# Kernel optimization log

Measured on AMD Instinct MI355X. Metric: run time of the kernel, lower is better.

## Reference

```python
import jax, jax.numpy as jnp
import numpy as np

B, N, F, H, OUT = 64, 512, 128, 256, 6


def setup_inputs() -> dict:
    key = jax.random.key(0)
    ks = jax.random.split(key, 20)
    s = 0.02
    inp = {
        "x": jax.random.normal(ks[0], (B * N, F), dtype=jnp.float32),
        "edge_index": jax.random.randint(ks[1], (2, 16), 0, B * N),
        "edge_weight": jax.random.uniform(ks[2], (16,), dtype=jnp.float32),
        "batch": jnp.repeat(jnp.arange(B, dtype=jnp.int64), N),
        "sigma": jax.random.uniform(ks[3], (1,), dtype=jnp.float32),
        "Wg": s * jax.random.normal(ks[4], (F, F)), "bg": jnp.zeros((F,)),
        "Wrel0": s * jax.random.normal(ks[5], (F, H)), "Wroot0": s * jax.random.normal(ks[6], (F, H)), "brel0": jnp.zeros((H,)),
        "Wrel1": s * jax.random.normal(ks[7], (H, H)), "Wroot1": s * jax.random.normal(ks[8], (H, H)), "brel1": jnp.zeros((H,)),
        "Wrel2": s * jax.random.normal(ks[9], (H, H)), "Wroot2": s * jax.random.normal(ks[10], (H, H)), "brel2": jnp.zeros((H,)),
        "W1": s * jax.random.normal(ks[11], (H, H)), "b1": jnp.zeros((H,)),
        "Wout": s * jax.random.normal(ks[12], (H, OUT)), "bout": jnp.zeros((OUT,)),
    }
    return inp


def _forward(x, sigma, Wg, bg, Wrel0, Wroot0, brel0, Wrel1, Wroot1, brel1,
             Wrel2, Wroot2, brel2, W1, b1, Wout, bout):
    # gdmLinear
    h = x @ Wg + bg                      # [B*N, F]
    hw = h.reshape(B, N, -1)             # to_dense_batch (equal-size windows)
    # pairwise squared distances per window -> Gaussian kernel
    sq = jnp.sum(hw * hw, axis=-1)       # [B, N]
    dist = jnp.maximum(sq[:, :, None] + sq[:, None, :]
                       - 2.0 * jnp.einsum('bnf,bmf->bnm', hw, hw), 0.0)
    A = jnp.exp(-dist / (2.0 * sigma[0] ** 2))   # [B, N, N], all > 0
    A = A * (1.0 - jnp.eye(N, dtype=A.dtype))    # nonzero extraction drops self-loops

    def conv(h, Wrel, Wroot, brel):
        # GraphConv: out_i = W_rel @ sum_j A[j,i] * h_j + b_rel + W_root @ h_i
        agg = jnp.einsum('bji,bjf->bif', A, h)
        return agg @ Wrel + brel + h @ Wroot

    h = hw
    h = jax.nn.relu(conv(h, Wrel0, Wroot0, brel0))
    h = jax.nn.relu(conv(h, Wrel1, Wroot1, brel1))
    h = conv(h, Wrel2, Wroot2, brel2)
    g = jnp.mean(h, axis=1)              # global_mean_pool (equal-size graphs)
    g = jax.nn.relu(g @ W1 + b1)
    return g @ Wout + bout               # [B, OUT]


def reference(x, edge_index, edge_weight, batch, sigma, Wg, bg,
              Wrel0, Wroot0, brel0, Wrel1, Wroot1, brel1,
              Wrel2, Wroot2, brel2, W1, b1, Wout, bout):
    # edge_index / edge_weight / batch inputs are recomputed internally by GdmGNN
    return _forward(x, sigma, Wg, bg, Wrel0, Wroot0, brel0, Wrel1, Wroot1, brel1,
                    Wrel2, Wroot2, brel2, W1, b1, Wout, bout)
```

## Files before the change

### kernel.cpp

```cpp
#include <hip/hip_runtime.h>
#include <math.h>

#define Bsz 64
#define Nn 512
#define Ff 128
#define Hh 256
#define OUTD 6

typedef __bf16 bf16x8 __attribute__((ext_vector_type(8)));
typedef float f32x4 __attribute__((ext_vector_type(4)));
typedef unsigned short ushort4v __attribute__((ext_vector_type(4)));

__device__ __forceinline__ unsigned short f2bf(float f) {
    unsigned u = __float_as_uint(f);
    u += 0x7FFFu + ((u >> 16) & 1u);
    return (unsigned short)(u >> 16);
}
__device__ __forceinline__ float bf2f(unsigned short s) {
    return __uint_as_float(((unsigned)s) << 16);
}

#define SWZ(r) (((r) ^ ((r) >> 2)) & 3)

__device__ __forceinline__ void async_ld16(const unsigned short* g, unsigned short* l) {
    __builtin_amdgcn_global_load_lds(
        (const __attribute__((address_space(1))) void*)g,
        (__attribute__((address_space(3))) void*)l,
        16, 0, 0);
}

__device__ __forceinline__ void wait_vm(int n) {
    switch (n) {
        case 0: asm volatile("s_waitcnt vmcnt(0)" ::: "memory"); break;
        case 1: asm volatile("s_waitcnt vmcnt(1)" ::: "memory"); break;
        case 2: asm volatile("s_waitcnt vmcnt(2)" ::: "memory"); break;
        case 3: asm volatile("s_waitcnt vmcnt(3)" ::: "memory"); break;
        case 4: asm volatile("s_waitcnt vmcnt(4)" ::: "memory"); break;
        case 5: asm volatile("s_waitcnt vmcnt(5)" ::: "memory"); break;
        default: asm volatile("s_waitcnt vmcnt(6)" ::: "memory"); break;
    }
}
__device__ __forceinline__ void pipe_barrier(int n) {
    wait_vm(n);
    __builtin_amdgcn_s_barrier();
    __builtin_amdgcn_sched_barrier(0);
}
__device__ __forceinline__ void drain_barrier() { pipe_barrier(0); }

#define LDH 40
#define TSZ (128 * 32)
#define ATS (256 * 32)

__device__ __forceinline__ int tsw_idx(int kt, int nl, int fo) {
    return kt * 4096 + nl * 32 + ((((fo >> 3) & 3) ^ SWZ(nl)) << 3) + (fo & 7);
}

__global__ __launch_bounds__(512) void fused_l0_gram(
    const unsigned short* __restrict__ h0b,
    const unsigned short* __restrict__ h0T,
    const unsigned short* __restrict__ WrelT0,
    const unsigned short* __restrict__ WrootT0,
    const float* __restrict__ brel0,
    const float* __restrict__ sqv, const float* __restrict__ sigma,
    unsigned short* __restrict__ Aadj,
    float* __restrict__ w,
    unsigned short* __restrict__ h1b,
    unsigned short* __restrict__ h1T)
{
    int id = blockIdx.x;
    int b = id & 63;
    int nt = id >> 6;
    int n0g = nt * 128;
    long nodeBase = (long)b * Nn + n0g;

    const unsigned short* HT = h0T + (long)b * Ff * Nn;
    const float* SQ = sqv + (long)b * Nn;
    unsigned short* Ab = Aadj + (long)b * Nn * Nn;

    __shared__ __align__(16) unsigned char SMEM[123392];
    unsigned short* H0R = (unsigned short*)(SMEM);
    unsigned short* H0C = (unsigned short*)(SMEM + 32768);
    unsigned short* ACH = (unsigned short*)(SMEM + 65536);
    unsigned short* SAh = (unsigned short*)(SMEM + 98304);
    float* rsum = (float*)(SMEM + 122880);
    unsigned short* AGK = (unsigned short*)(SMEM);
    unsigned short* SA2 = (unsigned short*)(SMEM + 32768);
    unsigned short* SB2 = (unsigned short*)(SMEM + 81920);

    int tid = threadIdx.x;
    int lane = tid & 63;
    int wave = tid >> 6;
    int quad = lane >> 4, l16 = lane & 15;
    int sr = lane >> 2, sc = lane & 3;

    float sg = sigma[0];
    float inv2s2 = 1.0f / (2.0f * sg * sg);

    auto issueH0R = [&]() {
        int r = wave * 16 + sr;
        int c = sc ^ SWZ(r);
        #pragma unroll
        for (int kt = 0; kt < 4; ++kt)
            async_ld16(h0b + (nodeBase + r) * Ff + kt * 32 + c * 8,
                       H0R + kt * 4096 + (wave * 16) * 32);
    };
    auto issueH0C = [&](int kc) {
        const unsigned short* src = h0b + ((long)b * Nn + kc * 128) * Ff;
        int r = wave * 16 + sr;
        int c = sc ^ SWZ(r);
        #pragma unroll
        for (int kt = 0; kt < 4; ++kt)
            async_ld16(src + (long)r * Ff + kt * 32 + c * 8,
                       H0C + kt * 4096 + (wave * 16) * 32);
    };
    auto issueHT = [&](int g) {
        int r = wave * 16 + sr;
        int c = sc ^ SWZ(r);
        async_ld16(HT + (long)r * Nn + g * 32 + c * 8,
                   SAh + (g % 3) * 4096 + (wave * 16) * 32);
    };

    int wmS = (wave >> 1) * 32, wnS = (wave & 1) * 64;
    f32x4 accS1[2][4] = {};
    int wmG = (wave >> 1) * 32, wnG = (wave & 1) * 64;

    if (tid < 128) rsum[tid] = 0.f;
    issueH0R();
    issueH0C(0);
    issueHT(0);

    for (int kc = 0; kc < 4; ++kc) {
        drain_barrier();

        f32x4 gr[2][4] = {};
        #pragma unroll
        for (int ks = 0; ks < 4; ++ks) {
            bf16x8 af[2], bfr[4];
            #pragma unroll
            for (int i = 0; i < 2; ++i) {
                int r = wmG + i * 16 + l16;
                af[i] = *(const bf16x8*)&H0C[ks * 4096 + r * 32 + (quad ^ SWZ(r)) * 8];
            }
            #pragma unroll
            for (int j = 0; j < 4; ++j) {
                int r = wnG + j * 16 + l16;
                bfr[j] = *(const bf16x8*)&H0R[ks * 4096 + r * 32 + (quad ^ SWZ(r)) * 8];
            }
            #pragma unroll
            for (int i = 0; i < 2; ++i)
                #pragma unroll
                for (int j = 0; j < 4; ++j)
                    gr[i][j] = __builtin_amdgcn_mfma_f32_16x16x32_bf16(
                        af[i], bfr[j], gr[i][j], 0, 0, 0);
        }

        {
            float ws0 = 0.f, ws1 = 0.f, ws2 = 0.f, ws3 = 0.f;
            #pragma unroll
            for (int i = 0; i < 2; ++i) {
                int krow = wmG + i * 16 + quad * 4;
                int ktl = krow >> 5, fol = krow & 31;
                #pragma unroll
                for (int j = 0; j < 4; ++j) {
                    int n = wnG + j * 16 + l16;
                    int nglob = n0g + n;
                    float sqn = SQ[nglob];
                    f32x4 v = gr[i][j];
                    ushort4v pk;
                    float asum = 0.f;
                    #pragma unroll
                    for (int r4 = 0; r4 < 4; ++r4) {
                        int kglob = kc * 128 + krow + r4;
                        float d = fmaxf(sqn + SQ[kglob] - 2.0f * v[r4], 0.0f);
                        unsigned short a = (nglob == kglob) ? (unsigned short)0
                                                            : f2bf(__expf(-d * inv2s2));
                        pk[r4] = a;
                        asum += bf2f(a);
                    }
                    *(ushort4v*)&ACH[ktl * 4096 + n * 32 +
                                     ((((fol >> 3) ^ SWZ(n)) << 3) + (fol & 7))] = pk;
                    *(ushort4v*)&Ab[(long)nglob * Nn + kc * 128 + krow] = pk;
                    if (j == 0) ws0 += asum;
                    else if (j == 1) ws1 += asum;
                    else if (j == 2) ws2 += asum;
                    else ws3 += asum;
                }
            }
            #pragma unroll
            for (int j = 0; j < 4; ++j) {
                float cs = (j == 0) ? ws0 : (j == 1) ? ws1 : (j == 2) ? ws2 : ws3;
                cs += __shfl_xor(cs, 16);
                cs += __shfl_xor(cs, 32);
                if (lane < 16)
                    atomicAdd(&rsum[wnG + j * 16 + l16], cs);
            }
        }
        __syncthreads();

        for (int t = 0; t < 4; ++t) {
            int g = kc * 4 + t;
            if (t < 3) issueHT(g + 1);
            else if (kc < 3) { issueH0C(kc + 1); issueHT(g + 1); }
            pipe_barrier(t < 3 ? 1 : (kc < 3 ? 5 : 0));
            const unsigned short* Abf = SAh + (g % 3) * 4096;
            bf16x8 af[2], bfr[4];
            #pragma unroll
            for (int i = 0; i < 2; ++i) {
                int r = wmS + i * 16 + l16;
                af[i] = *(const bf16x8*)&Abf[r * 32 + (quad ^ SWZ(r)) * 8];
            }
            #pragma unroll
            for (int j = 0; j < 4; ++j) {
                int nl = wnS + j * 16 + l16;
                bfr[j] = *(const bf16x8*)&ACH[tsw_idx(t, nl, quad * 8)];
            }
            #pragma unroll
            for (int i = 0; i < 2; ++i)
                #pragma unroll
                for (int j = 0; j < 4; ++j)
                    accS1[i][j] = __builtin_amdgcn_mfma_f32_16x16x32_bf16(
                        af[i], bfr[j], accS1[i][j], 0, 0, 0);
        }
    }

    #pragma unroll
    for (int i = 0; i < 2; ++i) {
        int f = wmS + i * 16 + quad * 4;
        int kt = f >> 5, fo = f & 31;
        #pragma unroll
        for (int j = 0; j < 4; ++j) {
            int nl = wnS + j * 16 + l16;
            f32x4 v = accS1[i][j];
            ushort4v p;
            p[0] = f2bf(v[0]); p[1] = f2bf(v[1]);
            p[2] = f2bf(v[2]); p[3] = f2bf(v[3]);
            *(ushort4v*)&AGK[tsw_idx(kt, nl, fo)] = p;
        }
    }
    __syncthreads();
    if (tid < 128) w[(long)b * Nn + n0g + tid] = rsum[tid];

    {
        int wm = (wave >> 1) * 64, wn = (wave & 1) * 64;
        f32x4 acc[4][4] = {};
        auto issue2 = [&](int g) {
            const unsigned short* Wp = (g < 4) ? WrelT0 : WrootT0;
            int kk = (g & 3) << 5;
            unsigned short* Ad = SA2 + (g % 3) * ATS;
            int r = wave * 16 + sr;
            int c = sc ^ SWZ(r);
            async_ld16(Wp + (long)r * Ff + kk + c * 8, Ad + (wave * 16) * 32);
            int r2 = 128 + r;
            int c2 = sc ^ SWZ(r2);
            async_ld16(Wp + (long)r2 * Ff + kk + c2 * 8, Ad + (128 + wave * 16) * 32);
            if (g >= 4) {
                unsigned short* Bd = SB2 + (g % 3) * TSZ;
                async_ld16(h0b + (nodeBase + r) * Ff + kk + c * 8,
                           Bd + (wave * 16) * 32);
            }
        };
        issue2(0); issue2(1);
        for (int g = 0; g < 8; ++g) {
            int nx = g + 1;
            pipe_barrier(nx >= 8 ? 0 : (nx < 4 ? 2 : 3));
            if (g + 2 < 8) issue2(g + 2);
            const unsigned short* Abf = SA2 + (g % 3) * ATS;
            bf16x8 af[4], bfr[4];
            #pragma unroll
            for (int i = 0; i < 4; ++i) {
                int r = wm + i * 16 + l16;
                af[i] = *(const bf16x8*)&Abf[r * 32 + (quad ^ SWZ(r)) * 8];
            }
            if (g < 4) {
                #pragma unroll
                for (int j = 0; j < 4; ++j) {
                    int nl = wn + j * 16 + l16;
                    bfr[j] = *(const bf16x8*)&AGK[tsw_idx(g, nl, quad * 8)];
                }
            } else {
                const unsigned short* Bb = SB2 + (g % 3) * TSZ;
                #pragma unroll
                for (int j = 0; j < 4; ++j) {
                    int r = wn + j * 16 + l16;
                    bfr[j] = *(const bf16x8*)&Bb[r * 32 + (quad ^ SWZ(r)) * 8];
                }
            }
            #pragma unroll
            for (int i = 0; i < 4; ++i)
                #pragma unroll
                for (int j = 0; j < 4; ++j)
                    acc[i][j] = __builtin_amdgcn_mfma_f32_16x16x32_bf16(
                        af[i], bfr[j], acc[i][j], 0, 0, 0);
        }
        #pragma unroll
        for (int i = 0; i < 4; ++i) {
            int of = wm + i * 16 + quad * 4;
            float b0 = brel0[of + 0], b1 = brel0[of + 1];
            float b2 = brel0[of + 2], b3 = brel0[of + 3];
            #pragma unroll
            for (int j = 0; j < 4; ++j) {
                int nl = wn + j * 16 + l16;
                f32x4 v = acc[i][j];
                float o0 = fmaxf(v[0] + b0, 0.f), o1 = fmaxf(v[1] + b1, 0.f);
                float o2 = fmaxf(v[2] + b2, 0.f), o3 = fmaxf(v[3] + b3, 0.f);
                ushort4v p;
                p[0] = f2bf(o0); p[1] = f2bf(o1); p[2] = f2bf(o2); p[3] = f2bf(o3);
                *(ushort4v*)&h1b[(nodeBase + nl) * Hh + of] = p;
                long base = ((long)b * Hh) * 512 + n0g + nl;
                h1T[base + (long)(of + 0) * 512] = p[0];
                h1T[base + (long)(of + 1) * 512] = p[1];
                h1T[base + (long)(of + 2) * 512] = p[2];
                h1T[base + (long)(of + 3) * 512] = p[3];
            }
        }
    }
}

__global__ __launch_bounds__(512) void fused_l1(
    const unsigned short* __restrict__ h1T,
    const unsigned short* __restrict__ Arows,
    const unsigned short* __restrict__ h1b,
    const unsigned short* __restrict__ WrelT1,
    const unsigned short* __restrict__ WrootT1,
    const float* __restrict__ brel1,
    const float* __restrict__ w,
    float* __restrict__ vpart, float* __restrict__ mpart)
{
    constexpr int BTS = 128 * 32;

    int id = blockIdx.x;
    int b = id & 63;
    int nt = id >> 6;
    int n0g = nt * 128;
    long nodeBase = (long)b * Nn + n0g;

    const unsigned short* HT = h1T + (long)b * Hh * Nn;
    const unsigned short* AR = Arows + (long)b * Nn * Nn;

    __shared__ unsigned short SA[3 * ATS];
    __shared__ unsigned short SB[3 * BTS];
    __shared__ unsigned short AGK[8 * 128 * 32];

    int tid = threadIdx.x;
    int lane = tid & 63;
    int wave = tid >> 6;
    int quad = lane >> 4, l16 = lane & 15;
    int wm = (wave >> 1) * 64;
    int wn = (wave & 1) * 64;
    int sr = lane >> 2, sc = lane & 3;

    {
        f32x4 acc[4][4] = {};
        auto issue = [&](int g) {
            int kk = g << 5;
            unsigned short* Ad = SA + (g % 3) * ATS;
            int r = wave * 16 + sr;
            int c = sc ^ SWZ(r);
            async_ld16(HT + (long)r * Nn + kk + c * 8, Ad + (wave * 16) * 32);
            int r2 = 128 + r;
            int c2 = sc ^ SWZ(r2);
            async_ld16(HT + (long)r2 * Nn + kk + c2 * 8, Ad + (128 + wave * 16) * 32);
            unsigned short* Bd = SB + (g % 3) * BTS;
            async_ld16(AR + (long)(n0g + r) * Nn + kk + c * 8, Bd + (wave * 16) * 32);
        };
        issue(0); issue(1);
        for (int g = 0; g < 16; ++g) {
            pipe_barrier(g + 1 < 16 ? 3 : 0);
            if (g + 2 < 16) issue(g + 2);
            const unsigned short* Ab = SA + (g % 3) * ATS;
            const unsigned short* Bb = SB + (g % 3) * BTS;
            bf16x8 af[4], bfr[4];
            #pragma unroll
            for (int i = 0; i < 4; ++i) {
                int r = wm + i * 16 + l16;
                af[i] = *(const bf16x8*)&Ab[r * 32 + (quad ^ SWZ(r)) * 8];
            }
            #pragma unroll
            for (int j = 0; j < 4; ++j) {
                int r = wn + j * 16 + l16;
                bfr[j] = *(const bf16x8*)&Bb[r * 32 + (quad ^ SWZ(r)) * 8];
            }
            #pragma unroll
            for (int i = 0; i < 4; ++i)
                #pragma unroll
                for (int j = 0; j < 4; ++j)
                    acc[i][j] = __builtin_amdgcn_mfma_f32_16x16x32_bf16(
                        af[i], bfr[j], acc[i][j], 0, 0, 0);
        }
        #pragma unroll
        for (int i = 0; i < 4; ++i) {
            int f = wm + i * 16 + quad * 4;
            int kt = f >> 5, fo = f & 31;
            #pragma unroll
            for (int j = 0; j < 4; ++j) {
                int nl = wn + j * 16 + l16;
                f32x4 v = acc[i][j];
                ushort4v p;
                p[0] = f2bf(v[0]); p[1] = f2bf(v[1]);
                p[2] = f2bf(v[2]); p[3] = f2bf(v[3]);
                *(ushort4v*)&AGK[tsw_idx(kt, nl, fo)] = p;
            }
        }
    }
    __syncthreads();

    f32x4 acc[4][4] = {};
    auto issue2 = [&](int g) {
        const unsigned short* Wp = (g < 8) ? WrelT1 : WrootT1;
        int kk = (g & 7) << 5;
        unsigned short* Ad = SA + (g % 3) * ATS;
        int r = wave * 16 + sr;
        int c = sc ^ SWZ(r);
        async_ld16(Wp + (long)r * Hh + kk + c * 8, Ad + (wave * 16) * 32);
        int r2 = 128 + r;
        int c2 = sc ^ SWZ(r2);
        async_ld16(Wp + (long)r2 * Hh + kk + c2 * 8, Ad + (128 + wave * 16) * 32);
        if (g >= 8) {
            unsigned short* Bd = SB + (g % 3) * BTS;
            async_ld16(h1b + (nodeBase + r) * Hh + kk + c * 8, Bd + (wave * 16) * 32);
        }
    };
    issue2(0); issue2(1);
    for (int g = 0; g < 16; ++g) {
        int nx = g + 1;
        pipe_barrier(nx >= 16 ? 0 : (nx < 8 ? 2 : 3));
        if (g + 2 < 16) issue2(g + 2);
        const unsigned short* Ab = SA + (g % 3) * ATS;
        bf16x8 af[4], bfr[4];
        #pragma unroll
        for (int i = 0; i < 4; ++i) {
            int r = wm + i * 16 + l16;
            af[i] = *(const bf16x8*)&Ab[r * 32 + (quad ^ SWZ(r)) * 8];
        }
        if (g < 8) {
            #pragma unroll
            for (int j = 0; j < 4; ++j) {
                int nl = wn + j * 16 + l16;
                bfr[j] = *(const bf16x8*)&AGK[tsw_idx(g, nl, quad * 8)];
            }
        } else {
            const unsigned short* Bb = SB + (g % 3) * BTS;
            #pragma unroll
            for (int j = 0; j < 4; ++j) {
                int r = wn + j * 16 + l16;
                bfr[j] = *(const bf16x8*)&Bb[r * 32 + (quad ^ SWZ(r)) * 8];
            }
        }
        #pragma unroll
        for (int i = 0; i < 4; ++i)
            #pragma unroll
            for (int j = 0; j < 4; ++j)
                acc[i][j] = __builtin_amdgcn_mfma_f32_16x16x32_bf16(
                    af[i], bfr[j], acc[i][j], 0, 0, 0);
    }

    #pragma unroll
    for (int i = 0; i < 4; ++i) {
        int lf = wm + i * 16 + quad * 4;
        float b0 = brel1[lf + 0], b1 = brel1[lf + 1];
        float b2 = brel1[lf + 2], b3 = brel1[lf + 3];
        float vp0 = 0.f, vp1 = 0.f, vp2 = 0.f, vp3 = 0.f;
        float mp0 = 0.f, mp1 = 0.f, mp2 = 0.f, mp3 = 0.f;
        #pragma unroll
        for (int j = 0; j < 4; ++j) {
            long node = nodeBase + wn + j * 16 + l16;
            f32x4 v = acc[i][j];
            float o0 = fmaxf(v[0] + b0, 0.f), o1 = fmaxf(v[1] + b1, 0.f);
            float o2 = fmaxf(v[2] + b2, 0.f), o3 = fmaxf(v[3] + b3, 0.f);
            float h0v = bf2f(f2bf(o0)), h1v = bf2f(f2bf(o1));
            float h2v = bf2f(f2bf(o2)), h3v = bf2f(f2bf(o3));
            float wv = w[node];
            vp0 += wv * h0v; vp1 += wv * h1v; vp2 += wv * h2v; vp3 += wv * h3v;
            mp0 += h0v; mp1 += h1v; mp2 += h2v; mp3 += h3v;
        }
        #pragma unroll
        for (int m = 1; m < 16; m <<= 1) {
            vp0 += __shfl_xor(vp0, m); vp1 += __shfl_xor(vp1, m);
            vp2 += __shfl_xor(vp2, m); vp3 += __shfl_xor(vp3, m);
            mp0 += __shfl_xor(mp0, m); mp1 += __shfl_xor(mp1, m);
            mp2 += __shfl_xor(mp2, m); mp3 += __shfl_xor(mp3, m);
        }
        if (l16 == 0) {
            long o = ((long)(b * 8 + nt * 2 + (wave & 1))) * Hh + lf;
            float4 vv = {vp0, vp1, vp2, vp3};
            float4 mm = {mp0, mp1, mp2, mp3};
            *(float4*)&vpart[o] = vv;
            *(float4*)&mpart[o] = mm;
        }
    }
}

__global__ __launch_bounds__(256) void prep_h0(
    const float* __restrict__ x, const float* __restrict__ Wg,
    const float* __restrict__ bg,
    const float* __restrict__ Wrel0, const float* __restrict__ Wroot0,
    const float* __restrict__ Wrel1, const float* __restrict__ Wroot1,
    unsigned short* __restrict__ T0, unsigned short* __restrict__ T1,
    unsigned short* __restrict__ T2, unsigned short* __restrict__ T3,
    float* __restrict__ w,
    unsigned short* __restrict__ h0b, unsigned short* __restrict__ h0T,
    float* __restrict__ sqv)
{
    if (blockIdx.x < 896) {
        int idx = blockIdx.x * 256 + threadIdx.x;
        if (idx >= 196608) { w[idx - 196608] = 0.f; return; }
        const float* src; unsigned short* dst; int kin; int e;
        if      (idx <  32768) { src = Wrel0;  dst = T0; kin = 128; e = idx; }
        else if (idx <  65536) { src = Wroot0; dst = T1; kin = 128; e = idx - 32768; }
        else if (idx < 131072) { src = Wrel1;  dst = T2; kin = 256; e = idx - 65536; }
        else                   { src = Wroot1; dst = T3; kin = 256; e = idx - 131072; }
        int o = (kin == 128) ? (e >> 7) : (e >> 8);
        int i = e & (kin - 1);
        dst[e] = f2bf(src[(long)i * 256 + o]);
        return;
    }

    __shared__ unsigned short As[128 * LDH];
    __shared__ unsigned short Bs[128 * LDH];
    __shared__ float rsq[128];

    int tid = threadIdx.x;
    int lane = tid & 63;
    int wave = tid >> 6;
    int quad = lane >> 4, l16 = lane & 15;
    int wm = (wave >> 1) * 64, wn = (wave & 1) * 64;
    int m0 = (blockIdx.x - 896) * 128;

    f32x4 acc[4][4] = {};

    for (int k0 = 0; k0 < Ff; k0 += 32) {
        __syncthreads();
        #pragma unroll
        for (int l = 0; l < 2; ++l) {
            int idx = tid + l * 256;
            int r = idx >> 2, ch = idx & 3;
            const float* px = x + (long)(m0 + r) * Ff + k0 + ch * 8;
            float4 xa = *(const float4*)px;
            float4 xb = *(const float4*)(px + 4);
            ushort4v pa, pb;
            pa[0] = f2bf(xa.x); pa[1] = f2bf(xa.y); pa[2] = f2bf(xa.z); pa[3] = f2bf(xa.w);
            pb[0] = f2bf(xb.x); pb[1] = f2bf(xb.y); pb[2] = f2bf(xb.z); pb[3] = f2bf(xb.w);
            *(ushort4v*)&As[r * LDH + ch * 8] = pa;
            *(ushort4v*)&As[r * LDH + ch * 8 + 4] = pb;
            int kk = k0 + ch * 8;
            ushort4v qa, qb;
            #pragma unroll
            for (int u = 0; u < 4; ++u) qa[u] = f2bf(Wg[(long)(kk + u) * 128 + r]);
            #pragma unroll
            for (int u = 0; u < 4; ++u) qb[u] = f2bf(Wg[(long)(kk + 4 + u) * 128 + r]);
            *(ushort4v*)&Bs[r * LDH + ch * 8] = qa;
            *(ushort4v*)&Bs[r * LDH + ch * 8 + 4] = qb;
        }
        __syncthreads();
        bf16x8 af[4], bfr[4];
        #pragma unroll
        for (int i = 0; i < 4; ++i)
            af[i] = *(const bf16x8*)&As[(wm + i * 16 + l16) * LDH + quad * 8];
        #pragma unroll
        for (int j = 0; j < 4; ++j)
            bfr[j] = *(const bf16x8*)&Bs[(wn + j * 16 + l16) * LDH + quad * 8];
        #pragma unroll
        for (int i = 0; i < 4; ++i)
            #pragma unroll
            for (int j = 0; j < 4; ++j)
                acc[i][j] = __builtin_amdgcn_mfma_f32_16x16x32_bf16(
                    af[i], bfr[j], acc[i][j], 0, 0, 0);
    }

    if (tid < 128) rsq[tid] = 0.f;
    __syncthreads();

    #pragma unroll
    for (int i = 0; i < 4; ++i) {
        int lrow = wm + i * 16 + quad * 4;
        int mb = m0 + lrow;
        float rp0 = 0.f, rp1 = 0.f, rp2 = 0.f, rp3 = 0.f;
        #pragma unroll
        for (int j = 0; j < 4; ++j) {
            int n = wn + j * 16 + l16;
            f32x4 v = acc[i][j];
            float bv = bg[n];
            unsigned short s0 = f2bf(v[0] + bv), s1 = f2bf(v[1] + bv);
            unsigned short s2 = f2bf(v[2] + bv), s3 = f2bf(v[3] + bv);
            h0b[(long)(mb + 0) * Ff + n] = s0;
            h0b[(long)(mb + 1) * Ff + n] = s1;
            h0b[(long)(mb + 2) * Ff + n] = s2;
            h0b[(long)(mb + 3) * Ff + n] = s3;
            ushort4v p; p[0] = s0; p[1] = s1; p[2] = s2; p[3] = s3;
            long ti = ((long)(mb >> 9) * Ff + n) * 512 + (mb & 511);
            *(ushort4v*)&h0T[ti] = p;
            float f0 = bf2f(s0), f1 = bf2f(s1), f2 = bf2f(s2), f3 = bf2f(s3);
            rp0 += f0 * f0; rp1 += f1 * f1; rp2 += f2 * f2; rp3 += f3 * f3;
        }
        #pragma unroll
        for (int m = 1; m < 16; m <<= 1) {
            rp0 += __shfl_xor(rp0, m);
            rp1 += __shfl_xor(rp1, m);
            rp2 += __shfl_xor(rp2, m);
            rp3 += __shfl_xor(rp3, m);
        }
        if (l16 == 0) {
            atomicAdd(&rsq[lrow + 0], rp0);
            atomicAdd(&rsq[lrow + 1], rp1);
            atomicAdd(&rsq[lrow + 2], rp2);
            atomicAdd(&rsq[lrow + 3], rp3);
        }
    }
    __syncthreads();
    if (tid < 128) sqv[m0 + tid] = rsq[tid];
}

__global__ __launch_bounds__(256) void head_kernel(
    const float* __restrict__ vpart, const float* __restrict__ mpart,
    const float* __restrict__ Wrel2, const float* __restrict__ Wroot2,
    const float* __restrict__ brel2,
    const float* __restrict__ W1, const float* __restrict__ b1,
    const float* __restrict__ Wout, const float* __restrict__ bout,
    float* __restrict__ out)
{
    int b = blockIdx.x;
    int j = threadIdx.x;
    __shared__ float vs[Hh], ms[Hh], gs[Hh], g2[Hh];
    float vp = 0.f, mp = 0.f;
    #pragma unroll
    for (int p = 0; p < 8; ++p) {
        long o = ((long)(b * 8 + p)) * Hh + j;
        vp += vpart[o];
        mp += mpart[o];
    }
    vs[j] = vp * (1.0f / (float)Nn);
    ms[j] = mp * (1.0f / (float)Nn);
    __syncthreads();
    float s = brel2[j];
    for (int c = 0; c < Hh; ++c)
        s += vs[c] * Wrel2[c * Hh + j] + ms[c] * Wroot2[c * Hh + j];
    gs[j] = s;
    __syncthreads();
    float t = b1[j];
    for (int k = 0; k < Hh; ++k) t += gs[k] * W1[k * Hh + j];
    g2[j] = fmaxf(t, 0.f);
    __syncthreads();
    if (j < OUTD) {
        float s2 = bout[j];
        for (int k = 0; k < Hh; ++k) s2 += g2[k] * Wout[k * OUTD + j];
        out[b * OUTD + j] = s2;
    }
}

extern "C" void kernel_launch(void* const* d_in, const int* in_sizes, int n_in,
                              void* d_out, int out_size, void* d_ws, size_t ws_size,
                              hipStream_t stream) {
    const float* x      = (const float*)d_in[0];
    const float* sigma  = (const float*)d_in[4];
    const float* Wg     = (const float*)d_in[5];
    const float* bg     = (const float*)d_in[6];
    const float* Wrel0  = (const float*)d_in[7];
    const float* Wroot0 = (const float*)d_in[8];
    const float* brel0  = (const float*)d_in[9];
    const float* Wrel1  = (const float*)d_in[10];
    const float* Wroot1 = (const float*)d_in[11];
    const float* brel1  = (const float*)d_in[12];
    const float* Wrel2  = (const float*)d_in[13];
    const float* Wroot2 = (const float*)d_in[14];
    const float* brel2  = (const float*)d_in[15];
    const float* W1     = (const float*)d_in[16];
    const float* b1     = (const float*)d_in[17];
    const float* Wout   = (const float*)d_in[18];
    const float* bout   = (const float*)d_in[19];
    float* out = (float*)d_out;

    char* ws = (char*)d_ws;
    unsigned short* h0b  = (unsigned short*)(ws + 16777216);
    unsigned short* h0T  = (unsigned short*)(ws + 25165824);
    float*          sq   = (float*)(ws + 33554432);
    unsigned short* Aadj = (unsigned short*)(ws + 33685504);
    unsigned short* h1b  = (unsigned short*)(ws + 84017152);
    unsigned short* h1T  = (unsigned short*)(ws + 100794368);
    unsigned short* WrelT0  = (unsigned short*)(ws + 167903232);
    unsigned short* WrootT0 = (unsigned short*)(ws + 167968768);
    unsigned short* WrelT1  = (unsigned short*)(ws + 168034304);
    unsigned short* WrootT1 = (unsigned short*)(ws + 168165376);
    float*          w     = (float*)(ws + 168558592);
    float*          vpart = (float*)(ws + 168689664);
    float*          mpart = (float*)(ws + 169213952);

    prep_h0<<<1152, 256, 0, stream>>>(x, Wg, bg, Wrel0, Wroot0, Wrel1, Wroot1,
                                      WrelT0, WrootT0, WrelT1, WrootT1,
                                      w, h0b, h0T, sq);

    fused_l0_gram<<<dim3(4 * Bsz, 1, 1), 512, 0, stream>>>(
        h0b, h0T, WrelT0, WrootT0, brel0, sq, sigma, Aadj, w, h1b, h1T);

    fused_l1<<<dim3(4 * Bsz, 1, 1), 512, 0, stream>>>(
        h1T, Aadj, h1b, WrelT1, WrootT1, brel1, w, vpart, mpart);

    head_kernel<<<Bsz, 256, 0, stream>>>(vpart, mpart, Wrel2, Wroot2, brel2,
                                         W1, b1, Wout, bout, out);
}
```

Baseline: 206.7 us.

## Recompute Gaussian adjacency in layer-1 kernel instead of storing to global

Layer 0 no longer writes the dense bf16 adjacency matrix (64x512x512) to global memory. Layer 1 instead recomputes each 128-column chunk of A from h0 with a Gram MFMA and an exp, then feeds it from LDS into the aggregation GEMM. This trades about 32 MB of global writes and reads for extra matrix and exp work plus larger LDS use (144 KB), which could limit occupancy.

Measured after the change: 208.2 us. No clear change (+0.7%).

```diff
diff --git a/kernel.cpp b/kernel.cpp
--- a/kernel.cpp
+++ b/kernel.cpp
@@ -62,7 +62,6 @@
     const unsigned short* __restrict__ WrootT0,
     const float* __restrict__ brel0,
     const float* __restrict__ sqv, const float* __restrict__ sigma,
-    unsigned short* __restrict__ Aadj,
     float* __restrict__ w,
     unsigned short* __restrict__ h1b,
     unsigned short* __restrict__ h1T)
@@ -75,7 +74,6 @@
 
     const unsigned short* HT = h0T + (long)b * Ff * Nn;
     const float* SQ = sqv + (long)b * Nn;
-    unsigned short* Ab = Aadj + (long)b * Nn * Nn;
 
     __shared__ __align__(16) unsigned char SMEM[123392];
     unsigned short* H0R = (unsigned short*)(SMEM);
@@ -179,7 +177,6 @@
                     }
                     *(ushort4v*)&ACH[ktl * 4096 + n * 32 +
                                      ((((fol >> 3) ^ SWZ(n)) << 3) + (fol & 7))] = pk;
-                    *(ushort4v*)&Ab[(long)nglob * Nn + kc * 128 + krow] = pk;
                     if (j == 0) ws0 += asum;
                     else if (j == 1) ws1 += asum;
                     else if (j == 2) ws2 += asum;
@@ -316,18 +313,17 @@
     }
 }
 
-__global__ __launch_bounds__(512) void fused_l1(
+__global__ __launch_bounds__(512) void fused_l1_gram(
     const unsigned short* __restrict__ h1T,
-    const unsigned short* __restrict__ Arows,
+    const unsigned short* __restrict__ h0b,
     const unsigned short* __restrict__ h1b,
     const unsigned short* __restrict__ WrelT1,
     const unsigned short* __restrict__ WrootT1,
     const float* __restrict__ brel1,
+    const float* __restrict__ sqv, const float* __restrict__ sigma,
     const float* __restrict__ w,
     float* __restrict__ vpart, float* __restrict__ mpart)
 {
-    constexpr int BTS = 128 * 32;
-
     int id = blockIdx.x;
     int b = id & 63;
     int nt = id >> 6;
@@ -335,71 +331,148 @@
     long nodeBase = (long)b * Nn + n0g;
 
     const unsigned short* HT = h1T + (long)b * Hh * Nn;
-    const unsigned short* AR = Arows + (long)b * Nn * Nn;
-
-    __shared__ unsigned short SA[3 * ATS];
-    __shared__ unsigned short SB[3 * BTS];
-    __shared__ unsigned short AGK[8 * 128 * 32];
+    const float* SQ = sqv + (long)b * Nn;
+
+    __shared__ __align__(16) unsigned char SMEM[147456];
+    unsigned short* H0R = (unsigned short*)(SMEM);
+    unsigned short* H0C = (unsigned short*)(SMEM + 32768);
+    unsigned short* ACH = (unsigned short*)(SMEM + 65536);
+    unsigned short* SAh = (unsigned short*)(SMEM + 98304);
+    unsigned short* AGK = (unsigned short*)(SMEM);
+    unsigned short* SA2 = (unsigned short*)(SMEM + 65536);
+    unsigned short* SB2 = (unsigned short*)(SMEM + 114688);
 
     int tid = threadIdx.x;
     int lane = tid & 63;
     int wave = tid >> 6;
     int quad = lane >> 4, l16 = lane & 15;
-    int wm = (wave >> 1) * 64;
-    int wn = (wave & 1) * 64;
     int sr = lane >> 2, sc = lane & 3;
 
-    {
-        f32x4 acc[4][4] = {};
-        auto issue = [&](int g) {
-            int kk = g << 5;
-            unsigned short* Ad = SA + (g % 3) * ATS;
-            int r = wave * 16 + sr;
-            int c = sc ^ SWZ(r);
-            async_ld16(HT + (long)r * Nn + kk + c * 8, Ad + (wave * 16) * 32);
-            int r2 = 128 + r;
-            int c2 = sc ^ SWZ(r2);
-            async_ld16(HT + (long)r2 * Nn + kk + c2 * 8, Ad + (128 + wave * 16) * 32);
-            unsigned short* Bd = SB + (g % 3) * BTS;
-            async_ld16(AR + (long)(n0g + r) * Nn + kk + c * 8, Bd + (wave * 16) * 32);
-        };
-        issue(0); issue(1);
-        for (int g = 0; g < 16; ++g) {
-            pipe_barrier(g + 1 < 16 ? 3 : 0);
-            if (g + 2 < 16) issue(g + 2);
-            const unsigned short* Ab = SA + (g % 3) * ATS;
-            const unsigned short* Bb = SB + (g % 3) * BTS;
+    float sg = sigma[0];
+    float inv2s2 = 1.0f / (2.0f * sg * sg);
+
+    auto issueH0R = [&]() {
+        int r = wave * 16 + sr;
+        int c = sc ^ SWZ(r);
+        #pragma unroll
+        for (int kt = 0; kt < 4; ++kt)
+            async_ld16(h0b + (nodeBase + r) * Ff + kt * 32 + c * 8,
+                       H0R + kt * 4096 + (wave * 16) * 32);
+    };
+    auto issueH0C = [&](int kc) {
+        const unsigned short* src = h0b + ((long)b * Nn + kc * 128) * Ff;
+        int r = wave * 16 + sr;
+        int c = sc ^ SWZ(r);
+        #pragma unroll
+        for (int kt = 0; kt < 4; ++kt)
+            async_ld16(src + (long)r * Ff + kt * 32 + c * 8,
+                       H0C + kt * 4096 + (wave * 16) * 32);
+    };
+    auto issueHT = [&](int g) {
+        int r = wave * 16 + sr;
+        int c = sc ^ SWZ(r);
+        unsigned short* Ad = SAh + (g % 3) * ATS;
+        async_ld16(HT + (long)r * Nn + g * 32 + c * 8, Ad + (wave * 16) * 32);
+        int r2 = 128 + r;
+        int c2 = sc ^ SWZ(r2);
+        async_ld16(HT + (long)r2 * Nn + g * 32 + c2 * 8, Ad + (128 + wave * 16) * 32);
+    };
+
+    int wmS = (wave >> 1) * 64, wnS = (wave & 1) * 64;
+    int wmG = (wave >> 1) * 32, wnG = (wave & 1) * 64;
+    f32x4 accS[4][4] = {};
+
+    issueH0R();
+    issueH0C(0);
+    issueHT(0);
+
+    for (int kc = 0; kc < 4; ++kc) {
+        drain_barrier();
+
+        f32x4 gr[2][4] = {};
+        #pragma unroll
+        for (int ks = 0; ks < 4; ++ks) {
+            bf16x8 af[2], bfr[4];
+            #pragma unroll
+            for (int i = 0; i < 2; ++i) {
+                int r = wmG + i * 16 + l16;
+                af[i] = *(const bf16x8*)&H0C[ks * 4096 + r * 32 + (quad ^ SWZ(r)) * 8];
+            }
+            #pragma unroll
+            for (int j = 0; j < 4; ++j) {
+                int r = wnG + j * 16 + l16;
+                bfr[j] = *(const bf16x8*)&H0R[ks * 4096 + r * 32 + (quad ^ SWZ(r)) * 8];
+            }
+            #pragma unroll
+            for (int i = 0; i < 2; ++i)
+                #pragma unroll
+                for (int j = 0; j < 4; ++j)
+                    gr[i][j] = __builtin_amdgcn_mfma_f32_16x16x32_bf16(
+                        af[i], bfr[j], gr[i][j], 0, 0, 0);
+        }
+
+        #pragma unroll
+        for (int i = 0; i < 2; ++i) {
+            int krow = wmG + i * 16 + quad * 4;
+            int ktl = krow >> 5, fol = krow & 31;
+            #pragma unroll
+            for (int j = 0; j < 4; ++j) {
+                int n = wnG + j * 16 + l16;
+                int nglob = n0g + n;
+                float sqn = SQ[nglob];
+                f32x4 v = gr[i][j];
+                ushort4v pk;
+                #pragma unroll
+                for (int r4 = 0; r4 < 4; ++r4) {
+                    int kglob = kc * 128 + krow + r4;
+                    float d = fmaxf(sqn + SQ[kglob] - 2.0f * v[r4], 0.0f);
+                    pk[r4] = (nglob == kglob) ? (unsigned short)0
+                                              : f2bf(__expf(-d * inv2s2));
+                }
+                *(ushort4v*)&ACH[ktl * 4096 + n * 32 +
+                                 ((((fol >> 3) ^ SWZ(n)) << 3) + (fol & 7))] = pk;
+            }
+        }
+        __syncthreads();
+
+        for (int t = 0; t < 4; ++t) {
+            int g = kc * 4 + t;
+            if (t < 3) issueHT(g + 1);
+            else if (kc < 3) { issueH0C(kc + 1); issueHT(g + 1); }
+            pipe_barrier(t < 3 ? 2 : (kc < 3 ? 6 : 0));
+            const unsigned short* Abf = SAh + (g % 3) * ATS;
             bf16x8 af[4], bfr[4];
             #pragma unroll
             for (int i = 0; i < 4; ++i) {
-                int r = wm + i * 16 + l16;
-                af[i] = *(const bf16x8*)&Ab[r * 32 + (quad ^ SWZ(r)) * 8];
-            }
-            #pragma unroll
-            for (int j = 0; j < 4; ++j) {
-                int r = wn + j * 16 + l16;
-                bfr[j] = *(const bf16x8*)&Bb[r * 32 + (quad ^ SWZ(r)) * 8];
+                int r = wmS + i * 16 + l16;
+                af[i] = *(const bf16x8*)&Abf[r * 32 + (quad ^ SWZ(r)) * 8];
+            }
+            #pragma unroll
+            for (int j = 0; j < 4; ++j) {
+                int nl = wnS + j * 16 + l16;
+                bfr[j] = *(const bf16x8*)&ACH[tsw_idx(t, nl, quad * 8)];
             }
             #pragma unroll
             for (int i = 0; i < 4; ++i)
                 #pragma unroll
                 for (int j = 0; j < 4; ++j)
-                    acc[i][j] = __builtin_amdgcn_mfma_f32_16x16x32_bf16(
-                        af[i], bfr[j], acc[i][j], 0, 0, 0);
-        }
-        #pragma unroll
-        for (int i = 0; i < 4; ++i) {
-            int f = wm + i * 16 + quad * 4;
-            int kt = f >> 5, fo = f & 31;
-            #pragma unroll
-            for (int j = 0; j < 4; ++j) {
-                int nl = wn + j * 16 + l16;
-                f32x4 v = acc[i][j];
-                ushort4v p;
-                p[0] = f2bf(v[0]); p[1] = f2bf(v[1]);
-                p[2] = f2bf(v[2]); p[3] = f2bf(v[3]);
-                *(ushort4v*)&AGK[tsw_idx(kt, nl, fo)] = p;
-            }
+                    accS[i][j] = __builtin_amdgcn_mfma_f32_16x16x32_bf16(
+                        af[i], bfr[j], accS[i][j], 0, 0, 0);
+        }
+    }
+
+    #pragma unroll
+    for (int i = 0; i < 4; ++i) {
+        int f = wmS + i * 16 + quad * 4;
+        int kt = f >> 5, fo = f & 31;
+        #pragma unroll
+        for (int j = 0; j < 4; ++j) {
+            int nl = wnS + j * 16 + l16;
+            f32x4 v = accS[i][j];
+            ushort4v p;
+            p[0] = f2bf(v[0]); p[1] = f2bf(v[1]);
+            p[2] = f2bf(v[2]); p[3] = f2bf(v[3]);
+            *(ushort4v*)&AGK[tsw_idx(kt, nl, fo)] = p;
         }
     }
     __syncthreads();
@@ -408,7 +481,7 @@
     auto issue2 = [&](int g) {
         const unsigned short* Wp = (g < 8) ? WrelT1 : WrootT1;
         int kk = (g & 7) << 5;
-        unsigned short* Ad = SA + (g % 3) * ATS;
+        unsigned short* Ad = SA2 + (g % 3) * ATS;
         int r = wave * 16 + sr;
         int c = sc ^ SWZ(r);
         async_ld16(Wp + (long)r * Hh + kk + c * 8, Ad + (wave * 16) * 32);
@@ -416,7 +489,7 @@
         int c2 = sc ^ SWZ(r2);
         async_ld16(Wp + (long)r2 * Hh + kk + c2 * 8, Ad + (128 + wave * 16) * 32);
         if (g >= 8) {
-            unsigned short* Bd = SB + (g % 3) * BTS;
+            unsigned short* Bd = SB2 + (g % 3) * TSZ;
             async_ld16(h1b + (nodeBase + r) * Hh + kk + c * 8, Bd + (wave * 16) * 32);
         }
     };
@@ -425,24 +498,24 @@
         int nx = g + 1;
         pipe_barrier(nx >= 16 ? 0 : (nx < 8 ? 2 : 3));
         if (g + 2 < 16) issue2(g + 2);
-        const unsigned short* Ab = SA + (g % 3) * ATS;
+        const unsigned short* Ab = SA2 + (g % 3) * ATS;
         bf16x8 af[4], bfr[4];
         #pragma unroll
         for (int i = 0; i < 4; ++i) {
-            int r = wm + i * 16 + l16;
+            int r = wmS + i * 16 + l16;
             af[i] = *(const bf16x8*)&Ab[r * 32 + (quad ^ SWZ(r)) * 8];
         }
         if (g < 8) {
             #pragma unroll
             for (int j = 0; j < 4; ++j) {
-                int nl = wn + j * 16 + l16;
+                int nl = wnS + j * 16 + l16;
                 bfr[j] = *(const bf16x8*)&AGK[tsw_idx(g, nl, quad * 8)];
             }
         } else {
-            const unsigned short* Bb = SB + (g % 3) * BTS;
-            #pragma unroll
-            for (int j = 0; j < 4; ++j) {
-                int r = wn + j * 16 + l16;
+            const unsigned short* Bb = SB2 + (g % 3) * TSZ;
+            #pragma unroll
+            for (int j = 0; j < 4; ++j) {
+                int r = wnS + j * 16 + l16;
                 bfr[j] = *(const bf16x8*)&Bb[r * 32 + (quad ^ SWZ(r)) * 8];
             }
         }
@@ -456,14 +529,14 @@
 
     #pragma unroll
     for (int i = 0; i < 4; ++i) {
-        int lf = wm + i * 16 + quad * 4;
+        int lf = wmS + i * 16 + quad * 4;
         float b0 = brel1[lf + 0], b1 = brel1[lf + 1];
         float b2 = brel1[lf + 2], b3 = brel1[lf + 3];
         float vp0 = 0.f, vp1 = 0.f, vp2 = 0.f, vp3 = 0.f;
         float mp0 = 0.f, mp1 = 0.f, mp2 = 0.f, mp3 = 0.f;
         #pragma unroll
         for (int j = 0; j < 4; ++j) {
-            long node = nodeBase + wn + j * 16 + l16;
+            long node = nodeBase + wnS + j * 16 + l16;
             f32x4 v = acc[i][j];
             float o0 = fmaxf(v[0] + b0, 0.f), o1 = fmaxf(v[1] + b1, 0.f);
             float o2 = fmaxf(v[2] + b2, 0.f), o3 = fmaxf(v[3] + b3, 0.f);
@@ -673,7 +746,6 @@
     unsigned short* h0b  = (unsigned short*)(ws + 16777216);
     unsigned short* h0T  = (unsigned short*)(ws + 25165824);
     float*          sq   = (float*)(ws + 33554432);
-    unsigned short* Aadj = (unsigned short*)(ws + 33685504);
     unsigned short* h1b  = (unsigned short*)(ws + 84017152);
     unsigned short* h1T  = (unsigned short*)(ws + 100794368);
     unsigned short* WrelT0  = (unsigned short*)(ws + 167903232);
@@ -689,10 +761,10 @@
                                       w, h0b, h0T, sq);
 
     fused_l0_gram<<<dim3(4 * Bsz, 1, 1), 512, 0, stream>>>(
-        h0b, h0T, WrelT0, WrootT0, brel0, sq, sigma, Aadj, w, h1b, h1T);
-
-    fused_l1<<<dim3(4 * Bsz, 1, 1), 512, 0, stream>>>(
-        h1T, Aadj, h1b, WrelT1, WrootT1, brel1, w, vpart, mpart);
+        h0b, h0T, WrelT0, WrootT0, brel0, sq, sigma, w, h1b, h1T);
+
+    fused_l1_gram<<<dim3(4 * Bsz, 1, 1), 512, 0, stream>>>(
+        h1T, h0b, h1b, WrelT1, WrootT1, brel1, sq, sigma, w, vpart, mpart);
 
     head_kernel<<<Bsz, 256, 0, stream>>>(vpart, mpart, Wrel2, Wroot2, brel2,
                                          W1, b1, Wout, bout, out);
```
